# Performance work log

Measured on AMD Instinct MI355X. Metric: run time of the kernel, lower is better.

## Reference

```python
import jax, jax.numpy as jnp
import numpy as np

VOCAB, F, H1, H2 = 64, 4096, 64, 32   # vocab size, featureVectorSize, hidden dims (hard-coded 64/32/1 in source)
NBBOX, NWORDS = 8192, 16


def _uniform(key, shape, fan_in):
    # torch nn.Linear default init: U(-1/sqrt(fan_in), 1/sqrt(fan_in))
    bound = 1.0 / np.sqrt(fan_in)
    return jax.random.uniform(key, shape, jnp.float32, -bound, bound)


def setup_inputs() -> dict:
    key = jax.random.key(0)
    ks = jax.random.split(key, 8)
    x = jax.random.normal(ks[0], (NBBOX, F), jnp.float32)
    words = jax.random.randint(ks[1], (NWORDS,), 0, VOCAB)  # indices of active word-models
    # Stacked per-word MLP params (one tiny MLP per vocab word)
    W1 = _uniform(ks[2], (VOCAB, F, H1), F)
    b1 = _uniform(ks[3], (VOCAB, H1), F)
    W2 = _uniform(ks[4], (VOCAB, H1, H2), H1)
    b2 = _uniform(ks[5], (VOCAB, H2), H1)
    W3 = _uniform(ks[6], (VOCAB, H2), H2)   # Linear(32,1) weight, squeezed to [VOCAB, H2]
    b3 = _uniform(ks[7], (VOCAB,), H2)
    return {"nBBox": NBBOX, "x": x, "words": words,
            "W1": W1, "b1": b1, "W2": W2, "b2": b2, "W3": W3, "b3": b3}


def reference(nBBox, x, words, W1, b1, W2, b2, W3, b3):
    # Gather the active word-models (dict lookup in the original)
    w1, c1 = W1[words], b1[words]          # [W,F,H1], [W,H1]
    w2, c2 = W2[words], b2[words]          # [W,H1,H2], [W,H2]
    w3, c3 = W3[words], b3[words]          # [W,H2], [W]
    # Batched 3-layer MLP over all active words at once (replaces Python loop)
    h1 = jax.nn.relu(jnp.einsum('bf,wfh->wbh', x, w1) + c1[:, None, :])   # [W,B,H1]
    h2 = jax.nn.relu(jnp.einsum('wbh,whk->wbk', h1, w2) + c2[:, None, :])  # [W,B,H2]
    logits = jnp.einsum('wbk,wk->wb', h2, w3) + c3[:, None]                # [W,B]
    # output = ones(nBBox,1) * prod_w sigmoid(logits_w)
    return jnp.prod(jax.nn.sigmoid(logits), axis=0)[:, None]               # [B,1]
```

## Files before the change

kernel.cpp:

```cpp
#include <hip/hip_runtime.h>
#include <stdint.h>
#include <math.h>

#define NBBOX 8192
#define FDIM  4096
#define H1DIM 64
#define H2DIM 32
#define NW    16
#define NCOL  1024

typedef __attribute__((ext_vector_type(8))) _Float16 f16x8;
typedef __attribute__((ext_vector_type(4))) float    f32x4;

typedef __attribute__((address_space(1))) void* gptr_t;
typedef __attribute__((address_space(3))) void* lptr_t;

__device__ __forceinline__ void g2l16(const void* g, void* l) {
    __builtin_amdgcn_global_load_lds((gptr_t)(uintptr_t)g,
                                     (lptr_t)(uint32_t)(uintptr_t)l,
                                     16, 0, 0);
}

__global__ __launch_bounds__(256) void prep(
    const float* __restrict__ x, _Float16* __restrict__ xh,
    const float* __restrict__ W1, const int* __restrict__ words,
    uint32_t* __restrict__ bth_u32)
{
    __shared__ uint32_t t[64 * 69];
    const int tid = threadIdx.x;

    if (blockIdx.x >= 512) {
        const int gid = (blockIdx.x - 512) * 256 + tid;
        const int idx = gid * 8;
        float4 a = *(const float4*)(x + idx);
        float4 b = *(const float4*)(x + idx + 4);
        f16x8 h;
        h[0] = (_Float16)a.x; h[1] = (_Float16)a.y; h[2] = (_Float16)a.z; h[3] = (_Float16)a.w;
        h[4] = (_Float16)b.x; h[5] = (_Float16)b.y; h[6] = (_Float16)b.z; h[7] = (_Float16)b.w;
        *(f16x8*)(xh + idx) = h;
        return;
    }

    const int wi = blockIdx.x >> 5;
    const int ft = blockIdx.x & 31;
    const int f0 = ft * 128;
    const int w  = words[wi];
    const int c    = tid & 63;
    const int fgrp = tid >> 6;

    const float* src = W1 + ((size_t)w * FDIM + f0) * H1DIM + c;
#pragma unroll
    for (int p = 0; p < 16; ++p) {
        const int f = fgrp * 2 + p * 8;
        float v0 = src[(size_t)f * H1DIM];
        float v1 = src[(size_t)(f + 1) * H1DIM];
        union { _Float16 h[2]; uint32_t u; } pk;
        pk.h[0] = (_Float16)v0; pk.h[1] = (_Float16)v1;
        t[c * 69 + (f >> 1)] = pk.u;
    }
    __syncthreads();
#pragma unroll
    for (int p = 0; p < 16; ++p) {
        const int cc = p * 4 + (tid >> 6);
        const int fd = tid & 63;
        bth_u32[(size_t)(wi * 64 + cc) * (FDIM / 2) + ft * 64 + fd] = t[cc * 69 + fd];
    }
}

__global__ __launch_bounds__(256, 2) void gemm_fused(
    const _Float16* __restrict__ xh, const _Float16* __restrict__ bth,
    const float* __restrict__ b1, const int* __restrict__ words,
    const float* __restrict__ W2, const float* __restrict__ b2,
    const float* __restrict__ W3, const float* __restrict__ b3,
    float* __restrict__ sig)
{
    __shared__ __align__(16) char smem[65536];
    _Float16 (*As)[128 * 32] = (_Float16 (*)[128 * 32])smem;
    _Float16 (*Bs)[128 * 32] = (_Float16 (*)[128 * 32])(smem + 16384);
    float* tile = (float*)smem;

    const int mt   = blockIdx.x & 63;
    const int nt   = blockIdx.x >> 6;
    const int t    = threadIdx.x;
    const int w    = t >> 6;
    const int lane = t & 63;
    const int m0 = mt * 128, n0 = nt * 128;

    f32x4 acc[4][4] = {};

    const int rs = w * 16 + (lane >> 2);
    const int kc = (lane & 3) * 8;

    const _Float16* A = xh  + (size_t)m0 * FDIM;
    const _Float16* B = bth + (size_t)n0 * FDIM;

    const int wm = w >> 1, wn = w & 1;
    const int ml = lane & 15;
    const int q8 = (lane >> 4) * 8;

    for (int kt = 0; kt < 64; ++kt) {
        const int k0 = kt * 64;
#pragma unroll
        for (int s = 0; s < 2; ++s) {
            const int kp = k0 + s * 32 + kc;
            g2l16(A + (size_t)rs * FDIM + kp,        &As[s][w * 512]);
            g2l16(A + (size_t)(rs + 64) * FDIM + kp, &As[s][2048 + w * 512]);
            g2l16(B + (size_t)rs * FDIM + kp,        &Bs[s][w * 512]);
            g2l16(B + (size_t)(rs + 64) * FDIM + kp, &Bs[s][2048 + w * 512]);
        }
        __syncthreads();

#pragma unroll
        for (int s = 0; s < 2; ++s) {
            f16x8 af[4], bfr[4];
#pragma unroll
            for (int i = 0; i < 4; ++i)
                af[i] = *(const f16x8*)&As[s][(wm * 64 + i * 16 + ml) * 32 + q8];
#pragma unroll
            for (int j = 0; j < 4; ++j)
                bfr[j] = *(const f16x8*)&Bs[s][(wn * 64 + j * 16 + ml) * 32 + q8];
#pragma unroll
            for (int i = 0; i < 4; ++i)
#pragma unroll
                for (int j = 0; j < 4; ++j)
                    acc[i][j] = __builtin_amdgcn_mfma_f32_16x16x32_f16(af[i], bfr[j], acc[i][j], 0, 0, 0);
        }
        __syncthreads();
    }

    const int q  = lane >> 4;
    const int wi = nt * 2 + wn;
    const int wv = __builtin_amdgcn_readfirstlane(words[wi]);
    float* tw = tile + w * 4096;

#pragma unroll
    for (int j = 0; j < 4; ++j) {
        const int col = j * 16 + ml;
        const float bias = b1[wv * H1DIM + col];
        const int c = col >> 2, e = col & 3;
#pragma unroll
        for (int i = 0; i < 4; ++i) {
#pragma unroll
            for (int r = 0; r < 4; ++r) {
                const int row = i * 16 + q * 4 + r;
                const int pos = ((c + row) & 7) | (c & 8);
                float v = acc[i][j][r] + bias;
                tw[row * 64 + pos * 4 + e] = v > 0.f ? v : 0.f;
            }
        }
    }

    const float* W2w = W2 + (size_t)wv * (H1DIM * H2DIM);
    float a2[H2DIM];
#pragma unroll
    for (int j = 0; j < H2DIM; ++j) a2[j] = 0.f;

#pragma unroll
    for (int c2 = 0; c2 < 16; ++c2) {
        const int pos = ((c2 + lane) & 7) | (c2 & 8);
        f32x4 h = *(const f32x4*)&tw[lane * 64 + pos * 4];
#pragma unroll
        for (int kk = 0; kk < 4; ++kk) {
            const float hv = h[kk];
            const int k = c2 * 4 + kk;
#pragma unroll
            for (int j = 0; j < H2DIM; ++j)
                a2[j] = fmaf(hv, W2w[k * H2DIM + j], a2[j]);
        }
    }

    float logit = b3[wv];
#pragma unroll
    for (int j = 0; j < H2DIM; ++j) {
        float h2 = a2[j] + b2[wv * H2DIM + j];
        h2 = h2 > 0.f ? h2 : 0.f;
        logit = fmaf(h2, W3[wv * H2DIM + j], logit);
    }
    sig[(size_t)wi * NBBOX + m0 + wm * 64 + lane] = 1.f / (1.f + expf(-logit));
}

__global__ void prod_k(const float* __restrict__ sig, float* __restrict__ out) {
    const int r = blockIdx.x * 256 + threadIdx.x;
    float p = 1.f;
#pragma unroll
    for (int wi = 0; wi < NW; ++wi) p *= sig[(size_t)wi * NBBOX + r];
    out[r] = p;
}

extern "C" void kernel_launch(void* const* d_in, const int* in_sizes, int n_in,
                              void* d_out, int out_size, void* d_ws, size_t ws_size,
                              hipStream_t stream)
{
    const float* x   = (const float*)d_in[1];
    const int* words = (const int*)  d_in[2];
    const float* W1  = (const float*)d_in[3];
    const float* b1  = (const float*)d_in[4];
    const float* W2  = (const float*)d_in[5];
    const float* b2  = (const float*)d_in[6];
    const float* W3  = (const float*)d_in[7];
    const float* b3  = (const float*)d_in[8];
    float* out = (float*)d_out;

    char* ws = (char*)d_ws;
    _Float16* xh  = (_Float16*)(ws);
    _Float16* bth = (_Float16*)(ws + 67108864);
    float*    sig = (float*)   (ws + 67108864 + 8388608);

    prep<<<512 + NBBOX * FDIM / 8 / 256, 256, 0, stream>>>(x, xh, W1, words, (uint32_t*)bth);
    gemm_fused<<<512, 256, 0, stream>>>(xh, bth, b1, words, W2, b2, W3, b3, sig);
    prod_k<<<NBBOX / 256, 256, 0, stream>>>(sig, out);
}
```

Measured before the change: 327.4 us.

## Double-buffer GEMM tiles in LDS with XOR-swizzled layout

The main GEMM loop now prefetches the next K tile into a second LDS buffer while MFMAs consume the current one, so global-to-LDS loads overlap compute. The LDS layout changes to 64-half rows with an XOR swizzle on the 16-byte chunk index, meant to cut bank conflicts on the fragment reads. This drops one barrier per iteration but uses the full 64KB LDS, which may limit occupancy to the declared 2 blocks per CU.

```diff
diff --git a/kernel.cpp b/kernel.cpp
--- a/kernel.cpp
+++ b/kernel.cpp
@@ -7,7 +7,6 @@
 #define H1DIM 64
 #define H2DIM 32
 #define NW    16
-#define NCOL  1024
 
 typedef __attribute__((ext_vector_type(8))) _Float16 f16x8;
 typedef __attribute__((ext_vector_type(4))) float    f32x4;
@@ -75,8 +74,6 @@
     float* __restrict__ sig)
 {
     __shared__ __align__(16) char smem[65536];
-    _Float16 (*As)[128 * 32] = (_Float16 (*)[128 * 32])smem;
-    _Float16 (*Bs)[128 * 32] = (_Float16 (*)[128 * 32])(smem + 16384);
     float* tile = (float*)smem;
 
     const int mt   = blockIdx.x & 63;
@@ -88,37 +85,49 @@
 
     f32x4 acc[4][4] = {};
 
-    const int rs = w * 16 + (lane >> 2);
-    const int kc = (lane & 3) * 8;
-
-    const _Float16* A = xh  + (size_t)m0 * FDIM;
-    const _Float16* B = bth + (size_t)n0 * FDIM;
+    const int lr = lane >> 3;
+    const int cg = (lane & 7) ^ lr;
+    const _Float16* Ag = xh  + (size_t)(m0 + w * 32 + lr) * FDIM + cg * 8;
+    const _Float16* Bg = bth + (size_t)(n0 + w * 32 + lr) * FDIM + cg * 8;
+    const int ldst = w * 32 * 128;
 
     const int wm = w >> 1, wn = w & 1;
     const int ml = lane & 15;
-    const int q8 = (lane >> 4) * 8;
-
+    const int qw = lane >> 4;
+
+#pragma unroll
+    for (int c = 0; c < 4; ++c) {
+        g2l16(Ag + (size_t)(c * 8) * FDIM, smem + ldst + c * 1024);
+        g2l16(Bg + (size_t)(c * 8) * FDIM, smem + 16384 + ldst + c * 1024);
+    }
+    __syncthreads();
+
+    int cur = 0;
     for (int kt = 0; kt < 64; ++kt) {
-        const int k0 = kt * 64;
-#pragma unroll
-        for (int s = 0; s < 2; ++s) {
-            const int kp = k0 + s * 32 + kc;
-            g2l16(A + (size_t)rs * FDIM + kp,        &As[s][w * 512]);
-            g2l16(A + (size_t)(rs + 64) * FDIM + kp, &As[s][2048 + w * 512]);
-            g2l16(B + (size_t)rs * FDIM + kp,        &Bs[s][w * 512]);
-            g2l16(B + (size_t)(rs + 64) * FDIM + kp, &Bs[s][2048 + w * 512]);
-        }
-        __syncthreads();
-
+        if (kt < 63) {
+            const int nb = (cur ^ 1) * 32768;
+            const size_t ko = (size_t)(kt + 1) * 64;
+#pragma unroll
+            for (int c = 0; c < 4; ++c) {
+                g2l16(Ag + (size_t)(c * 8) * FDIM + ko, smem + nb + ldst + c * 1024);
+                g2l16(Bg + (size_t)(c * 8) * FDIM + ko, smem + nb + 16384 + ldst + c * 1024);
+            }
+        }
+        const _Float16* Ab = (const _Float16*)(smem + cur * 32768);
+        const _Float16* Bb = (const _Float16*)(smem + cur * 32768 + 16384);
 #pragma unroll
         for (int s = 0; s < 2; ++s) {
             f16x8 af[4], bfr[4];
 #pragma unroll
-            for (int i = 0; i < 4; ++i)
-                af[i] = *(const f16x8*)&As[s][(wm * 64 + i * 16 + ml) * 32 + q8];
-#pragma unroll
-            for (int j = 0; j < 4; ++j)
-                bfr[j] = *(const f16x8*)&Bs[s][(wn * 64 + j * 16 + ml) * 32 + q8];
+            for (int i = 0; i < 4; ++i) {
+                const int ra = wm * 64 + i * 16 + ml;
+                af[i] = *(const f16x8*)&Ab[ra * 64 + (((s * 4 + qw) ^ (ml & 7)) * 8)];
+            }
+#pragma unroll
+            for (int j = 0; j < 4; ++j) {
+                const int rb = wn * 64 + j * 16 + ml;
+                bfr[j] = *(const f16x8*)&Bb[rb * 64 + (((s * 4 + qw) ^ (ml & 7)) * 8)];
+            }
 #pragma unroll
             for (int i = 0; i < 4; ++i)
 #pragma unroll
@@ -126,6 +135,7 @@
                     acc[i][j] = __builtin_amdgcn_mfma_f32_16x16x32_f16(af[i], bfr[j], acc[i][j], 0, 0, 0);
         }
         __syncthreads();
+        cur ^= 1;
     }
 
     const int q  = lane >> 4;
```

Measured after the change: 317.5 us. 3.0% less time.
